# Optimization experiments

Measured on AMD Instinct MI355X. Metric: run time of the kernel, lower is better.

## Reference

```python
import jax, jax.numpy as jnp
import numpy as np

D_MODEL = 1024
D_HID = 1408
N_SHARED = 2
N_ROUTED = 8
TOP_K = 2
B, S = 2, 1024
EPS = float(jnp.finfo(jnp.float32).eps)  # torch RMSNorm eps=None -> finfo eps


def setup_inputs() -> dict:
    key = jax.random.key(0)
    ks = jax.random.split(key, 8)
    b1 = 1.0 / np.sqrt(D_MODEL)  # uniform bound for W1 (1/sqrt(d_input))
    b2 = 1.0 / np.sqrt(D_MODEL)  # uniform bound for W2 (1/sqrt(d_output))
    return {
        "x": jax.random.normal(ks[0], (B, S, D_MODEL), dtype=jnp.float32),
        "norm_w": jnp.ones((D_MODEL,), dtype=jnp.float32),
        "Wr": jax.random.uniform(ks[1], (N_ROUTED, D_MODEL), minval=-b1, maxval=b1, dtype=jnp.float32),
        "Ws1": jax.random.uniform(ks[2], (N_SHARED, D_MODEL, D_HID), minval=-b1, maxval=b1, dtype=jnp.float32),
        "bs1": jnp.zeros((N_SHARED, 1, D_HID), dtype=jnp.float32),
        "Ws2": jax.random.uniform(ks[3], (N_SHARED, D_HID, D_MODEL), minval=-b2, maxval=b2, dtype=jnp.float32),
        "bs2": jnp.zeros((N_SHARED, 1, D_MODEL), dtype=jnp.float32),
        "W1": jax.random.uniform(ks[4], (N_ROUTED, D_MODEL, D_HID), minval=-b1, maxval=b1, dtype=jnp.float32),
        "b1": jnp.zeros((N_ROUTED, 1, D_HID), dtype=jnp.float32),
        "W2": jax.random.uniform(ks[5], (N_ROUTED, D_HID, D_MODEL), minval=-b2, maxval=b2, dtype=jnp.float32),
        "b2": jnp.zeros((N_ROUTED, 1, D_MODEL), dtype=jnp.float32),
    }


def _rmsnorm(x, w):
    ms = jnp.mean(jnp.square(x), axis=-1, keepdims=True)
    return x * jax.lax.rsqrt(ms + EPS) * w


def reference(x, norm_w, Wr, Ws1, bs1, Ws2, bs2, W1, b1, W2, b2):
    inputs = _rmsnorm(x, norm_w)  # (B,S,d)

    # Shared experts: sum over all shared experts of SwiGLU-FFN
    hs = jax.nn.silu(jnp.einsum("bsd,edh->besh", inputs, Ws1) + bs1[:, None])  # (B,E_s,S,h)
    shared_out = jnp.einsum("besh,ehd->bsd", hs, Ws2) + jnp.sum(bs2[:, None], axis=0)  # (B,S,d)

    # Router (no bias, ver V2: affinity = raw logits)
    raw_aff = jnp.einsum("bsd,ed->bse", inputs, Wr)  # (B,S,E)
    _, idx = jax.lax.top_k(raw_aff, TOP_K)  # (B,S,K)

    # Routed experts: dropout=0, so computing all experts then gathering outputs
    # equals the source's per-token weight-gather math.
    hr = jax.nn.silu(jnp.einsum("bsd,edh->bseh", inputs, W1) + b1[:, 0])  # (B,S,E,h)
    out_all = jnp.einsum("bseh,ehd->bsed", hr, W2) + b2[:, 0]  # (B,S,E,d)

    out_k = jnp.take_along_axis(out_all, idx[..., None], axis=2)  # (B,S,K,d)
    aff_k = jnp.take_along_axis(raw_aff, idx, axis=-1)  # (B,S,K)
    routed_out = jnp.einsum("bsk,bskd->bsd", aff_k, out_k)

    return x + shared_out + routed_out
```

## Files before the change

kernel.cpp:

```cpp
#include <hip/hip_runtime.h>
#include <hip/hip_bf16.h>
#include <stdint.h>


#define NTOK 2048
#define DM   1024
#define DH   1408
#define DHP  1536
#define NGRP 10
#define EPSV 1.1920928955078125e-7f
#define MAXTILES 40
#define MAXSLOTS (MAXTILES * 256)

typedef __bf16 bf16x8 __attribute__((ext_vector_type(8)));
typedef float  f32x4  __attribute__((ext_vector_type(4)));
typedef unsigned short u16x8 __attribute__((ext_vector_type(8)));

__device__ __forceinline__ void async16(const void* g, void* l) {
  __builtin_amdgcn_global_load_lds(
      (const __attribute__((address_space(1))) unsigned*)g,
      (__attribute__((address_space(3))) unsigned*)l, 16, 0, 0);
}

__device__ __forceinline__ unsigned lds_off(const void* p) {
  return (unsigned)(unsigned long long)(const __attribute__((address_space(3))) char*)p;
}

__device__ __forceinline__ unsigned short f2bf(float f) {
  unsigned u = __builtin_bit_cast(unsigned, f);
  unsigned r = (u + 0x7FFFu + ((u >> 16) & 1u)) >> 16;
  return (unsigned short)r;
}
__device__ __forceinline__ float bf2f(unsigned short h) {
  unsigned u = ((unsigned)h) << 16;
  return __builtin_bit_cast(float, u);
}

__device__ __forceinline__ int xcd_swizzle(int id, int nwg) {
  int q = nwg >> 3;
  return (id & 7) * q + (id >> 3);
}

__global__ __launch_bounds__(256) void prep_k(
    const float* __restrict__ Ws1, const float* __restrict__ W1,
    const float* __restrict__ Ws2, const float* __restrict__ W2,
    unsigned short* __restrict__ W1t, unsigned short* __restrict__ W2t,
    const float* __restrict__ x, const float* __restrict__ nw,
    const float* __restrict__ Wr, unsigned short* __restrict__ xb,
    int* __restrict__ idx2, float* __restrict__ gate2) {
  __shared__ float tls[64][65];
  __shared__ float ps[4];
  __shared__ float pw[32];
  int bi = blockIdx.x;
  int tid = threadIdx.x;
  if (bi < 11520) {
    int z = bi / 576, rem = bi % 576, by = rem / 24, bx = rem % 24;
    const float* s; unsigned short* d; int C, dstride; bool zero = false;
    if (z < NGRP) {
      C = DH; dstride = DM;
      s = (z < 2) ? Ws1 + (size_t)z * DM * DH : W1 + (size_t)(z - 2) * DM * DH;
      d = W1t + (size_t)z * DHP * DM;
      if (by >= 16) return;
      zero = (bx >= 22);
    } else {
      int g = z - NGRP;
      C = DM; dstride = DH;
      s = (g < 2) ? Ws2 + (size_t)g * DH * DM : W2 + (size_t)(g - 2) * DH * DM;
      d = W2t + (size_t)g * DM * DH;
      if (bx >= 16 || by >= 22) return;
    }
    int r0 = by * 64, c0 = bx * 64;
    if (!zero) {
      int rr = tid >> 4, c4 = tid & 15;
#pragma unroll
      for (int p = 0; p < 4; ++p) {
        float4 v = *(const float4*)(s + (size_t)(r0 + p * 16 + rr) * C + c0 + c4 * 4);
        tls[p * 16 + rr][c4 * 4 + 0] = v.x;
        tls[p * 16 + rr][c4 * 4 + 1] = v.y;
        tls[p * 16 + rr][c4 * 4 + 2] = v.z;
        tls[p * 16 + rr][c4 * 4 + 3] = v.w;
      }
    }
    __syncthreads();
    int c = tid >> 2;
#pragma unroll
    for (int q = 0; q < 2; ++q) {
      int oct = (tid & 3) * 2 + q;
      u16x8 uv;
#pragma unroll
      for (int j = 0; j < 8; ++j) uv[j] = zero ? (unsigned short)0 : f2bf(tls[oct * 8 + j][c]);
      *(u16x8*)(d + (size_t)(c0 + c) * dstride + r0 + oct * 8) = uv;
    }
    return;
  }
  int t = bi - 11520;
  const float4 v = *(const float4*)(x + (size_t)t * DM + tid * 4);
  float s = v.x * v.x + v.y * v.y + v.z * v.z + v.w * v.w;
#pragma unroll
  for (int o = 32; o; o >>= 1) s += __shfl_down(s, o);
  if ((tid & 63) == 0) ps[tid >> 6] = s;
  __syncthreads();
  float tot = ps[0] + ps[1] + ps[2] + ps[3];
  float r = rsqrtf(tot * (1.0f / (float)DM) + EPSV);
  const float4 wv = *(const float4*)(nw + tid * 4);
  float4 y;
  y.x = v.x * r * wv.x; y.y = v.y * r * wv.y; y.z = v.z * r * wv.z; y.w = v.w * r * wv.w;
  ushort4 u; u.x = f2bf(y.x); u.y = f2bf(y.y); u.z = f2bf(y.z); u.w = f2bf(y.w);
  *(ushort4*)(xb + (size_t)t * DM + tid * 4) = u;
  float pr[8];
#pragma unroll
  for (int e = 0; e < 8; ++e) {
    const float4 w4 = *(const float4*)(Wr + (size_t)e * DM + tid * 4);
    pr[e] = y.x * w4.x + y.y * w4.y + y.z * w4.z + y.w * w4.w;
  }
#pragma unroll
  for (int e = 0; e < 8; ++e)
#pragma unroll
    for (int o = 32; o; o >>= 1) pr[e] += __shfl_down(pr[e], o);
  if ((tid & 63) == 0) {
    int w = tid >> 6;
#pragma unroll
    for (int e = 0; e < 8; ++e) pw[w * 8 + e] = pr[e];
  }
  __syncthreads();
  if (tid == 0) {
    float af[8];
#pragma unroll
    for (int e = 0; e < 8; ++e) af[e] = pw[e] + pw[8 + e] + pw[16 + e] + pw[24 + e];
    int e1 = 0; float a1 = af[0];
#pragma unroll
    for (int e = 1; e < 8; ++e) if (af[e] > a1) { a1 = af[e]; e1 = e; }
    int e2 = -1; float a2 = -3.4e38f;
#pragma unroll
    for (int e = 0; e < 8; ++e) if (e != e1 && af[e] > a2) { a2 = af[e]; e2 = e; }
    idx2[t * 2] = e1; idx2[t * 2 + 1] = e2;
    gate2[t * 2] = a1; gate2[t * 2 + 1] = a2;
  }
}

__global__ __launch_bounds__(256) void buildplace_k(
    const int* __restrict__ idx2, const float* __restrict__ gate2,
    const float* __restrict__ bs1, const float* __restrict__ b1,
    const float* __restrict__ bs2, const float* __restrict__ b2,
    int* __restrict__ tile_group, int* __restrict__ tok_list,
    float* __restrict__ gate_list, int* __restrict__ slot_of,
    float* __restrict__ b1p, float* __restrict__ b2p) {
  __shared__ int cnt_s[8], base_s[8], fill_s[8];
  int tid = threadIdx.x;
  if (tid < 8) { cnt_s[tid] = 0; fill_s[tid] = 0; }
  __syncthreads();
  for (int t = tid; t < NTOK; t += 256) {
    atomicAdd(&cnt_s[idx2[2 * t]], 1);
    atomicAdd(&cnt_s[idx2[2 * t + 1]], 1);
  }
  __syncthreads();
  if (tid == 0) {
    int tile = 16;
    for (int e = 0; e < 8; ++e) {
      base_s[e] = tile * 256;
      tile += (cnt_s[e] + 255) >> 8;
    }
    for (int i = 0; i < 16; ++i) tile_group[i] = i >> 3;
    int tt = 16;
    for (int e = 0; e < 8; ++e) {
      int nt = (cnt_s[e] + 255) >> 8;
      for (int i = 0; i < nt; ++i) tile_group[tt++] = 2 + e;
    }
    for (; tt < MAXTILES; ++tt) tile_group[tt] = -1;
  }
  for (int s = tid; s < MAXSLOTS; s += 256) {
    int tok; float gv;
    if (s < 2048)      { tok = s;        gv = 1.f; }
    else if (s < 4096) { tok = s - 2048; gv = 1.f; }
    else               { tok = -1;       gv = 0.f; }
    tok_list[s] = tok; gate_list[s] = gv;
  }
  for (int i = tid; i < NGRP * DH; i += 256) {
    int g = i / DH, j = i % DH;
    b1p[i] = (g < 2) ? bs1[g * DH + j] : b1[(g - 2) * DH + j];
  }
  for (int i = tid; i < NGRP * DM; i += 256) {
    int g = i >> 10, j = i & (DM - 1);
    b2p[i] = (g < 2) ? bs2[g * DM + j] : b2[(g - 2) * DM + j];
  }
  __syncthreads();
  for (int t = tid; t < NTOK; t += 256) {
#pragma unroll
    for (int k = 0; k < 2; ++k) {
      int e = idx2[t * 2 + k];
      int pos = atomicAdd(&fill_s[e], 1);
      int slot = base_s[e] + pos;
      tok_list[slot] = t;
      gate_list[slot] = gate2[t * 2 + k];
      slot_of[t * 2 + k] = slot;
    }
  }
}

#define DSR(dst, addr) asm volatile("ds_read_b128 %0, %1" : "=v"(dst) : "v"(addr))

template <int KD, int ND, int NBN, bool FIRST>
__global__ __launch_bounds__(512, 2) void gemm_k(
    const unsigned short* __restrict__ A, const int* __restrict__ tok_list,
    const int* __restrict__ tile_group, const unsigned short* __restrict__ Bt,
    const float* __restrict__ biasP, const float* __restrict__ gate_list,
    unsigned short* __restrict__ Out) {
  constexpr int NK = KD / 64;
  int wg = xcd_swizzle(blockIdx.x, MAXTILES * NBN);
  int tile = wg / NBN, bn = (wg % NBN) * 256;
  int g = tile_group[tile];
  if (g < 0) return;
  int tid = threadIdx.x;
  __shared__ unsigned short As[2][256 * 64];
  __shared__ unsigned short Bs[2][256 * 64];
  __shared__ int rows_s[256];
  __shared__ float gates_s[256];
  if (tid < 256) {
    if (FIRST) {
      int tok = tok_list[tile * 256 + tid];
      rows_s[tid] = tok < 0 ? 0 : tok;
    } else {
      gates_s[tid] = gate_list[tile * 256 + tid];
    }
  }
  __syncthreads();
  int drow = tid >> 3, schk = tid & 7, sxor = drow & 7;
  const unsigned short* aS[4];
  const unsigned short* bS[4];
#pragma unroll
  for (int p = 0; p < 4; ++p) {
    int rl = p * 64 + drow;
    int arow = FIRST ? rows_s[rl] : tile * 256 + rl;
    aS[p] = A + (size_t)arow * KD + (schk ^ sxor) * 8;
    bS[p] = Bt + ((size_t)g * ND + bn + rl) * KD + (schk ^ sxor) * 8;
  }
  int lane = tid & 63, w = tid >> 6;
  int wm = w >> 2, wn = w & 3;
  int lr = lane & 15, hi = lane >> 4;
  int aOff[8], bOff[4];
#pragma unroll
  for (int q = 0; q < 8; ++q) {
    int row = wm * 128 + (q >> 2) * 64 + (q & 3) * 16 + lr;
    aOff[q] = row * 128 + ((hi ^ (row & 7)) << 4);
  }
#pragma unroll
  for (int nf = 0; nf < 4; ++nf) {
    int row = wn * 64 + nf * 16 + lr;
    bOff[nf] = row * 128 + ((hi ^ (row & 7)) << 4);
  }
  unsigned aBase[2] = {lds_off(&As[0][0]), lds_off(&As[1][0])};
  unsigned bBase[2] = {lds_off(&Bs[0][0]), lds_off(&Bs[1][0])};
  f32x4 acc[8][4];
#pragma unroll
  for (int q = 0; q < 8; ++q)
#pragma unroll
    for (int nf = 0; nf < 4; ++nf) acc[q][nf] = (f32x4){0.f, 0.f, 0.f, 0.f};
  auto stage = [&](int buf, int kt) {
#pragma unroll
    for (int p = 0; p < 4; ++p) {
      async16(aS[p] + kt * 64, (char*)&As[buf][0] + p * 8192 + tid * 16);
      async16(bS[p] + kt * 64, (char*)&Bs[buf][0] + p * 8192 + tid * 16);
    }
  };
  stage(0, 0);
  int cur = 0;
  for (int kt = 0; kt < NK; ++kt) {
    if (kt + 1 < NK) {
      stage(cur ^ 1, kt + 1);
      asm volatile("s_waitcnt vmcnt(8)" ::: "memory");
    } else {
      asm volatile("s_waitcnt vmcnt(0)" ::: "memory");
    }
    asm volatile("s_barrier" ::: "memory");
#pragma unroll
    for (int ks = 0; ks < 2; ++ks) {
      int kx = ks ? 64 : 0;
      f32x4 ar[8], br[4];
#pragma unroll
      for (int q = 0; q < 8; ++q) {
        unsigned ad = aBase[cur] + (unsigned)(aOff[q] ^ kx);
        DSR(ar[q], ad);
      }
#pragma unroll
      for (int nf = 0; nf < 4; ++nf) {
        unsigned bd = bBase[cur] + (unsigned)(bOff[nf] ^ kx);
        DSR(br[nf], bd);
      }
      asm volatile("s_waitcnt lgkmcnt(0)" ::: "memory");
      __builtin_amdgcn_sched_barrier(0);
      __builtin_amdgcn_s_setprio(1);
#pragma unroll
      for (int q = 0; q < 8; ++q)
#pragma unroll
        for (int nf = 0; nf < 4; ++nf)
          acc[q][nf] = __builtin_amdgcn_mfma_f32_16x16x32_bf16(
              __builtin_bit_cast(bf16x8, ar[q]), __builtin_bit_cast(bf16x8, br[nf]),
              acc[q][nf], 0, 0, 0);
      __builtin_amdgcn_s_setprio(0);
    }
    asm volatile("s_barrier" ::: "memory");
    cur ^= 1;
  }
#pragma unroll
  for (int nf = 0; nf < 4; ++nf) {
    int col = bn + wn * 64 + nf * 16 + lr;
    if (!FIRST || col < DH) {
      float bv = biasP[g * (FIRST ? DH : DM) + col];
#pragma unroll
      for (int q = 0; q < 8; ++q) {
        int rl = wm * 128 + (q >> 2) * 64 + (q & 3) * 16 + hi * 4;
#pragma unroll
        for (int j = 0; j < 4; ++j) {
          float v = acc[q][nf][j] + bv;
          if (FIRST) {
            v = v / (1.f + expf(-v));
            Out[(size_t)(tile * 256 + rl + j) * DH + col] = f2bf(v);
          } else {
            v *= gates_s[rl + j];
            Out[(size_t)(tile * 256 + rl + j) * DM + col] = f2bf(v);
          }
        }
      }
    }
  }
}

__global__ __launch_bounds__(256) void combine_k(
    const float* __restrict__ x, const unsigned short* __restrict__ O,
    const int* __restrict__ slot_of, float* __restrict__ out) {
  int t = blockIdx.x, tid = threadIdx.x;
  int d = tid * 4;
  int s0 = slot_of[t * 2], s1 = slot_of[t * 2 + 1];
  float4 xv = *(const float4*)(x + (size_t)t * DM + d);
  ushort4 a = *(const ushort4*)(O + (size_t)t * DM + d);
  ushort4 b = *(const ushort4*)(O + (size_t)(2048 + t) * DM + d);
  ushort4 c = *(const ushort4*)(O + (size_t)s0 * DM + d);
  ushort4 e = *(const ushort4*)(O + (size_t)s1 * DM + d);
  float4 o;
  o.x = xv.x + bf2f(a.x) + bf2f(b.x) + bf2f(c.x) + bf2f(e.x);
  o.y = xv.y + bf2f(a.y) + bf2f(b.y) + bf2f(c.y) + bf2f(e.y);
  o.z = xv.z + bf2f(a.z) + bf2f(b.z) + bf2f(c.z) + bf2f(e.z);
  o.w = xv.w + bf2f(a.w) + bf2f(b.w) + bf2f(c.w) + bf2f(e.w);
  *(float4*)(out + (size_t)t * DM + d) = o;
}

extern "C" void kernel_launch(void* const* d_in, const int* in_sizes, int n_in,
                              void* d_out, int out_size, void* d_ws, size_t ws_size,
                              hipStream_t stream) {
  const float* x   = (const float*)d_in[0];
  const float* nw  = (const float*)d_in[1];
  const float* Wr  = (const float*)d_in[2];
  const float* Ws1 = (const float*)d_in[3];
  const float* bs1 = (const float*)d_in[4];
  const float* Ws2 = (const float*)d_in[5];
  const float* bs2 = (const float*)d_in[6];
  const float* W1  = (const float*)d_in[7];
  const float* b1  = (const float*)d_in[8];
  const float* W2  = (const float*)d_in[9];
  const float* b2  = (const float*)d_in[10];
  float* out = (float*)d_out;

  char* ws = (char*)d_ws;
  size_t off = 0;
  auto alloc = [&](size_t n) {
    size_t r = off;
    off += (n + 255) & ~(size_t)255;
    return r;
  };
  unsigned short* XnB  = (unsigned short*)(ws + alloc((size_t)NTOK * DM * 2));
  unsigned short* W1t  = (unsigned short*)(ws + alloc((size_t)NGRP * DHP * DM * 2));
  unsigned short* W2t  = (unsigned short*)(ws + alloc((size_t)NGRP * DM * DH * 2));
  unsigned short* Hb   = (unsigned short*)(ws + alloc((size_t)MAXSLOTS * DH * 2));
  unsigned short* Ob   = (unsigned short*)(ws + alloc((size_t)MAXSLOTS * DM * 2));
  int*   idx2      = (int*)(ws + alloc((size_t)NTOK * 2 * 4));
  float* gate2     = (float*)(ws + alloc((size_t)NTOK * 2 * 4));
  int*   tile_group= (int*)(ws + alloc(64 * 4));
  int*   tok_list  = (int*)(ws + alloc((size_t)MAXSLOTS * 4));
  float* gate_list = (float*)(ws + alloc((size_t)MAXSLOTS * 4));
  int*   slot_of   = (int*)(ws + alloc((size_t)NTOK * 2 * 4));
  float* b1p       = (float*)(ws + alloc((size_t)NGRP * DH * 4));
  float* b2p       = (float*)(ws + alloc((size_t)NGRP * DM * 4));

  prep_k<<<11520 + NTOK, 256, 0, stream>>>(Ws1, W1, Ws2, W2, W1t, W2t,
                                           x, nw, Wr, XnB, idx2, gate2);
  buildplace_k<<<1, 256, 0, stream>>>(idx2, gate2, bs1, b1, bs2, b2,
                                      tile_group, tok_list, gate_list, slot_of, b1p, b2p);
  gemm_k<DM, DHP, 6, true><<<MAXTILES * 6, 512, 0, stream>>>(
      XnB, tok_list, tile_group, W1t, b1p, nullptr, Hb);
  gemm_k<DH, DM, 4, false><<<MAXTILES * 4, 512, 0, stream>>>(
      Hb, tok_list, tile_group, W2t, b2p, gate_list, Ob);
  combine_k<<<NTOK, 256, 0, stream>>>(x, Ob, slot_of, out);
}
```

Baseline: 166.1 us.

## Use 128x128 bf16 LDS tiles for weight transpose and preload GEMM bias

The weight transpose/convert pass in prep_k now uses 128x128 tiles. Each tile is converted to bf16 before it is written to LDS, using an XOR swizzle to avoid bank conflicts. This replaces the 64x64 fp32 tiles and the many early-exit blocks, cutting the launch to 1840 transpose blocks and halving LDS traffic. The GEMM kernel also loads its bias values before the main loop and adds sched_barriers around the async staging, to pin the schedule and hide the bias load latency. The swizzled index math must be exactly right, and the extra scheduling barriers could constrain the compiler.

```diff
diff --git a/kernel.cpp b/kernel.cpp
--- a/kernel.cpp
+++ b/kernel.cpp
@@ -41,6 +41,7 @@
   return (id & 7) * q + (id >> 3);
 }
 
+#define TRN_BLKS 1840
 __global__ __launch_bounds__(256) void prep_k(
     const float* __restrict__ Ws1, const float* __restrict__ W1,
     const float* __restrict__ Ws2, const float* __restrict__ W2,
@@ -48,52 +49,58 @@
     const float* __restrict__ x, const float* __restrict__ nw,
     const float* __restrict__ Wr, unsigned short* __restrict__ xb,
     int* __restrict__ idx2, float* __restrict__ gate2) {
-  __shared__ float tls[64][65];
+  __shared__ unsigned short Lt[128 * 132];
   __shared__ float ps[4];
   __shared__ float pw[32];
   int bi = blockIdx.x;
   int tid = threadIdx.x;
-  if (bi < 11520) {
-    int z = bi / 576, rem = bi % 576, by = rem / 24, bx = rem % 24;
-    const float* s; unsigned short* d; int C, dstride; bool zero = false;
-    if (z < NGRP) {
-      C = DH; dstride = DM;
+  if (bi < TRN_BLKS) {
+    const float* s; unsigned short* d; int C, Kd, k0, n0; bool zero = false;
+    if (bi < 960) {
+      int z = bi / 96, rem = bi % 96, kb = rem / 12, nb = rem % 12;
+      C = DH; Kd = DM; k0 = kb * 128; n0 = nb * 128;
       s = (z < 2) ? Ws1 + (size_t)z * DM * DH : W1 + (size_t)(z - 2) * DM * DH;
       d = W1t + (size_t)z * DHP * DM;
-      if (by >= 16) return;
-      zero = (bx >= 22);
+      zero = (nb == 11);
     } else {
-      int g = z - NGRP;
-      C = DM; dstride = DH;
-      s = (g < 2) ? Ws2 + (size_t)g * DH * DM : W2 + (size_t)(g - 2) * DH * DM;
-      d = W2t + (size_t)g * DM * DH;
-      if (bx >= 16 || by >= 22) return;
-    }
-    int r0 = by * 64, c0 = bx * 64;
-    if (!zero) {
-      int rr = tid >> 4, c4 = tid & 15;
-#pragma unroll
-      for (int p = 0; p < 4; ++p) {
-        float4 v = *(const float4*)(s + (size_t)(r0 + p * 16 + rr) * C + c0 + c4 * 4);
-        tls[p * 16 + rr][c4 * 4 + 0] = v.x;
-        tls[p * 16 + rr][c4 * 4 + 1] = v.y;
-        tls[p * 16 + rr][c4 * 4 + 2] = v.z;
-        tls[p * 16 + rr][c4 * 4 + 3] = v.w;
+      int b2 = bi - 960;
+      int z = b2 / 88, rem = b2 % 88, kb = rem / 8, nb = rem % 8;
+      C = DM; Kd = DH; k0 = kb * 128; n0 = nb * 128;
+      s = (z < 2) ? Ws2 + (size_t)z * DH * DM : W2 + (size_t)(z - 2) * DH * DM;
+      d = W2t + (size_t)z * DM * DH;
+    }
+    if (zero) {
+      u16x8 uv = (u16x8){0, 0, 0, 0, 0, 0, 0, 0};
+#pragma unroll
+      for (int p = 0; p < 8; ++p) {
+        int n = p * 16 + (tid >> 4), kc = (tid & 15) * 8;
+        *(u16x8*)(d + (size_t)(n0 + n) * Kd + k0 + kc) = uv;
       }
+      return;
+    }
+#pragma unroll
+    for (int p = 0; p < 16; ++p) {
+      int kr = p * 8 + (tid >> 5);
+      int nc = (tid & 31) * 4;
+      float4 v = *(const float4*)(s + (size_t)(k0 + kr) * C + n0 + nc);
+      int ncs = nc ^ ((kr & 0x78) >> 1);
+      ushort4 u;
+      u.x = f2bf(v.x); u.y = f2bf(v.y); u.z = f2bf(v.z); u.w = f2bf(v.w);
+      *(ushort4*)(&Lt[kr * 132 + ncs]) = u;
     }
     __syncthreads();
-    int c = tid >> 2;
-#pragma unroll
-    for (int q = 0; q < 2; ++q) {
-      int oct = (tid & 3) * 2 + q;
+#pragma unroll
+    for (int p = 0; p < 8; ++p) {
+      int n = p * 16 + (tid >> 4), kc = (tid & 15) * 8;
+      int nswz = n ^ ((tid & 15) << 2);
       u16x8 uv;
 #pragma unroll
-      for (int j = 0; j < 8; ++j) uv[j] = zero ? (unsigned short)0 : f2bf(tls[oct * 8 + j][c]);
-      *(u16x8*)(d + (size_t)(c0 + c) * dstride + r0 + oct * 8) = uv;
+      for (int j = 0; j < 8; ++j) uv[j] = Lt[(kc + j) * 132 + nswz];
+      *(u16x8*)(d + (size_t)(n0 + n) * Kd + k0 + kc) = uv;
     }
     return;
   }
-  int t = bi - 11520;
+  int t = bi - TRN_BLKS;
   const float4 v = *(const float4*)(x + (size_t)t * DM + tid * 4);
   float s = v.x * v.x + v.y * v.y + v.z * v.z + v.w * v.w;
 #pragma unroll
@@ -250,6 +257,14 @@
   }
   unsigned aBase[2] = {lds_off(&As[0][0]), lds_off(&As[1][0])};
   unsigned bBase[2] = {lds_off(&Bs[0][0]), lds_off(&Bs[1][0])};
+  float bv[4];
+#pragma unroll
+  for (int nf = 0; nf < 4; ++nf) {
+    int col = bn + wn * 64 + nf * 16 + lr;
+    int cidx = (!FIRST || col < DH) ? col : 0;
+    bv[nf] = biasP[g * (FIRST ? DH : DM) + cidx];
+    asm volatile("" : "+v"(bv[nf]));
+  }
   f32x4 acc[8][4];
 #pragma unroll
   for (int q = 0; q < 8; ++q)
@@ -262,14 +277,21 @@
       async16(bS[p] + kt * 64, (char*)&Bs[buf][0] + p * 8192 + tid * 16);
     }
   };
+  asm volatile("s_waitcnt vmcnt(0)" ::: "memory");
+  __builtin_amdgcn_sched_barrier(0);
   stage(0, 0);
+  __builtin_amdgcn_sched_barrier(0);
   int cur = 0;
   for (int kt = 0; kt < NK; ++kt) {
     if (kt + 1 < NK) {
+      __builtin_amdgcn_sched_barrier(0);
       stage(cur ^ 1, kt + 1);
+      __builtin_amdgcn_sched_barrier(0);
       asm volatile("s_waitcnt vmcnt(8)" ::: "memory");
+      __builtin_amdgcn_sched_barrier(0);
     } else {
       asm volatile("s_waitcnt vmcnt(0)" ::: "memory");
+      __builtin_amdgcn_sched_barrier(0);
     }
     asm volatile("s_barrier" ::: "memory");
 #pragma unroll
@@ -305,13 +327,12 @@
   for (int nf = 0; nf < 4; ++nf) {
     int col = bn + wn * 64 + nf * 16 + lr;
     if (!FIRST || col < DH) {
-      float bv = biasP[g * (FIRST ? DH : DM) + col];
 #pragma unroll
       for (int q = 0; q < 8; ++q) {
         int rl = wm * 128 + (q >> 2) * 64 + (q & 3) * 16 + hi * 4;
 #pragma unroll
         for (int j = 0; j < 4; ++j) {
-          float v = acc[q][nf][j] + bv;
+          float v = acc[q][nf][j] + bv[nf];
           if (FIRST) {
             v = v / (1.f + expf(-v));
             Out[(size_t)(tile * 256 + rl + j) * DH + col] = f2bf(v);
@@ -381,8 +402,8 @@
   float* b1p       = (float*)(ws + alloc((size_t)NGRP * DH * 4));
   float* b2p       = (float*)(ws + alloc((size_t)NGRP * DM * 4));
 
-  prep_k<<<11520 + NTOK, 256, 0, stream>>>(Ws1, W1, Ws2, W2, W1t, W2t,
-                                           x, nw, Wr, XnB, idx2, gate2);
+  prep_k<<<TRN_BLKS + NTOK, 256, 0, stream>>>(Ws1, W1, Ws2, W2, W1t, W2t,
+                                              x, nw, Wr, XnB, idx2, gate2);
   buildplace_k<<<1, 256, 0, stream>>>(idx2, gate2, bs1, b1, bs2, b2,
                                       tile_group, tok_list, gate_list, slot_of, b1p, b2p);
   gemm_k<DM, DHP, 6, true><<<MAXTILES * 6, 512, 0, stream>>>(
```

Result: faster. 160.3 us (-3.5%).
